# Optimization experiments

Hardware: AMD Instinct MI355X
Metric: run time of the kernel (lower is better)

The kernel has to match this reference:

```python
import jax, jax.numpy as jnp
import numpy as np

NUM_HEADS = 32
HEAD_DIM = 128
HIDDEN = NUM_HEADS * HEAD_DIM  # 4096
ROPE_BASE = 10000.0
VISION_TOKEN_TYPE = 1


def vision_expert_mask(token_type_ids):
    # vision_token_mask[:, :-1] = (tt[:, :-1]==1) & (tt[:, 1:]==1); last col False
    tt = token_type_ids
    m = (tt[:, :-1] == VISION_TOKEN_TYPE) & (tt[:, 1:] == VISION_TOKEN_TYPE)
    return jnp.concatenate([m, jnp.zeros((tt.shape[0], 1), dtype=bool)], axis=1)


def rotary_cos_sin(position_ids, head_dim, dtype):
    inv_freq = 1.0 / (ROPE_BASE ** (jnp.arange(0, head_dim, 2, dtype=jnp.float32) / head_dim))
    freqs = position_ids.astype(jnp.float32)[..., None] * inv_freq  # [B,S,Dh/2]
    emb = jnp.concatenate([freqs, freqs], axis=-1)  # [B,S,Dh]
    return jnp.cos(emb).astype(dtype), jnp.sin(emb).astype(dtype)


def rotate_half(x):
    d = x.shape[-1] // 2
    return jnp.concatenate([-x[..., d:], x[..., :d]], axis=-1)


def setup_inputs() -> dict:
    key = jax.random.key(0)
    ks = jax.random.split(key, 5)
    B, S = 2, 2048
    hidden_states = jax.random.normal(ks[0], (B, S, HIDDEN), dtype=jnp.float32)
    token_type_ids = jax.random.randint(ks[1], (B, S), 0, 2, dtype=jnp.int64)
    position_ids = jnp.broadcast_to(jnp.arange(S, dtype=jnp.int64)[None, :], (B, S))
    scale = 0.02
    w_vis_qkv = jax.random.normal(ks[2], (HIDDEN, 3 * HIDDEN), dtype=jnp.float32) * scale
    w_lang_qkv = jax.random.normal(ks[3], (HIDDEN, 3 * HIDDEN), dtype=jnp.float32) * scale
    w_vis_dense = jax.random.normal(ks[4], (HIDDEN, HIDDEN), dtype=jnp.float32) * scale
    w_lang_dense = jax.random.normal(jax.random.fold_in(key, 7), (HIDDEN, HIDDEN), dtype=jnp.float32) * scale
    return dict(hidden_states=hidden_states, token_type_ids=token_type_ids,
                position_ids=position_ids, w_vis_qkv=w_vis_qkv, w_lang_qkv=w_lang_qkv,
                w_vis_dense=w_vis_dense, w_lang_dense=w_lang_dense)


def reference(hidden_states, token_type_ids, position_ids,
              w_vis_qkv, w_lang_qkv, w_vis_dense, w_lang_dense):
    B, S, D = hidden_states.shape
    vm = vision_expert_mask(token_type_ids)  # [B,S] bool

    # 2-expert QKV dispatch (mask-select between the two expert GEMMs)
    qkv = jnp.where(vm[..., None],
                    hidden_states @ w_vis_qkv,
                    hidden_states @ w_lang_qkv)  # [B,S,3D]
    q, k, v = jnp.split(qkv, 3, axis=-1)
    q = q.reshape(B, S, NUM_HEADS, HEAD_DIM)
    k = k.reshape(B, S, NUM_HEADS, HEAD_DIM)
    v = v.reshape(B, S, NUM_HEADS, HEAD_DIM)

    # rotary embedding on q, k
    cos, sin = rotary_cos_sin(position_ids, HEAD_DIM, q.dtype)  # [B,S,Dh]
    cos, sin = cos[:, :, None, :], sin[:, :, None, :]
    q = q * cos + rotate_half(q) * sin
    k = k * cos + rotate_half(k) * sin

    # causal attention (dense equivalent of the paged-attention call)
    scores = jnp.einsum('bqhd,bkhd->bhqk', q, k) / jnp.sqrt(jnp.array(HEAD_DIM, q.dtype))
    causal = jnp.tril(jnp.ones((S, S), dtype=bool))
    scores = jnp.where(causal[None, None], scores, jnp.finfo(scores.dtype).min)
    probs = jax.nn.softmax(scores, axis=-1)
    ctx = jnp.einsum('bhqk,bkhd->bqhd', probs, v).reshape(B, S, D)

    # 2-expert output dense dispatch
    attn_output = jnp.where(vm[..., None],
                            ctx @ w_vis_dense,
                            ctx @ w_lang_dense)
    return attn_output
```

## Files before the change

kernel.cpp:

```cpp
#include <hip/hip_runtime.h>
#include <math.h>

#define SEQ     2048
#define NB      2
#define NHEADS  32
#define DHEAD   128
#define HID     4096
#define NQKV    12288
#define T_TOKENS (NB*SEQ)

typedef _Float16 half8 __attribute__((ext_vector_type(8)));
typedef float v4f __attribute__((ext_vector_type(4)));

__device__ __forceinline__ void gload_lds16(const void* g, void* l) {
    __builtin_amdgcn_global_load_lds(
        (__attribute__((address_space(1))) void*)(void*)(g),
        (__attribute__((address_space(3))) void*)(unsigned)(unsigned long long)(l),
        16, 0, 0);
}

__device__ __forceinline__ v4f mfma16(half8 a, half8 b, v4f c) {
    return __builtin_amdgcn_mfma_f32_16x16x32_f16(a, b, c, 0, 0, 0);
}

__global__ void route_kernel(const int* __restrict__ tt, int* counts, int* idx) {
    int t = blockIdx.x * blockDim.x + threadIdx.x;
    if (t >= T_TOKENS) return;
    int s = t & (SEQ - 1);
    bool vm = (s < SEQ - 1) && (tt[t] == 1) && (tt[t + 1] == 1);
    int e = vm ? 0 : 1;
    int p = atomicAdd(&counts[e], 1);
    idx[e * T_TOKENS + p] = t;
}

__global__ void rope_table_kernel(const int* __restrict__ pos_ids, float2* __restrict__ tab) {
    int i = blockIdx.x * blockDim.x + threadIdx.x;
    if (i >= T_TOKENS * 64) return;
    int tok = i >> 6, j = i & 63;
    float invf = (float)pow(10000.0, -(double)j * (1.0 / 64.0));
    float ang = (float)pos_ids[tok] * invf;
    double ds, dc;
    sincos((double)ang, &ds, &dc);
    tab[i] = make_float2((float)dc, (float)ds);
}

__global__ void cvt_f32_f16(const float* __restrict__ src, _Float16* __restrict__ dst, int n4) {
    int i = blockIdx.x * blockDim.x + threadIdx.x;
    if (i >= n4) return;
    float4 v = ((const float4*)src)[i];
    union { _Float16 h[4]; uint2 u; } p;
    p.h[0] = (_Float16)v.x; p.h[1] = (_Float16)v.y;
    p.h[2] = (_Float16)v.z; p.h[3] = (_Float16)v.w;
    ((uint2*)dst)[i] = p.u;
}

__global__ void transpose_cvt(const float* __restrict__ W, _Float16* __restrict__ WT,
                              int K, int N) {
    __shared__ _Float16 t[64][72];
    const int n0 = blockIdx.x * 64, k0 = blockIdx.y * 64;
    const int cr = threadIdx.x & 15, rr = threadIdx.x >> 4;
#pragma unroll
    for (int it = 0; it < 4; ++it) {
        int r = rr + it * 16;
        float4 v = *(const float4*)&W[(size_t)(k0 + r) * N + n0 + cr * 4];
        t[cr*4+0][r] = (_Float16)v.x; t[cr*4+1][r] = (_Float16)v.y;
        t[cr*4+2][r] = (_Float16)v.z; t[cr*4+3][r] = (_Float16)v.w;
    }
    __syncthreads();
#pragma unroll
    for (int it = 0; it < 4; ++it) {
        int r = rr + it * 16;
        union { _Float16 h[4]; uint2 u; } p;
#pragma unroll
        for (int j = 0; j < 4; ++j) p.h[j] = t[r][cr*4+j];
        *(uint2*)&WT[(size_t)(n0 + r) * K + k0 + cr * 4] = p.u;
    }
}

__global__ void transpose_v(const _Float16* __restrict__ vin, _Float16* __restrict__ vout) {
    __shared__ _Float16 t[64][72];
    const int s0 = blockIdx.x * 64;
    const int d0 = blockIdx.y * 64;
    const int bh = blockIdx.z;
    const int b = bh >> 5, h = bh & 31;
    const int cr = threadIdx.x & 15, rr = threadIdx.x >> 4;
#pragma unroll
    for (int it = 0; it < 4; ++it) {
        int sl = rr + it * 16;
        union { _Float16 h4[4]; uint2 u; } p;
        p.u = *(const uint2*)&vin[(size_t)(b * SEQ + s0 + sl) * HID + h * DHEAD + d0 + cr * 4];
#pragma unroll
        for (int j = 0; j < 4; ++j) t[cr*4+j][sl] = p.h4[j];
    }
    __syncthreads();
#pragma unroll
    for (int it = 0; it < 4; ++it) {
        int dl = rr + it * 16;
        union { _Float16 h4[4]; uint2 u; } p;
#pragma unroll
        for (int j = 0; j < 4; ++j) p.h4[j] = t[dl][cr*4+j];
        *(uint2*)&vout[((size_t)bh * DHEAD + d0 + dl) * SEQ + s0 + cr * 4] = p.u;
    }
}

template <int MODE>
__global__ __launch_bounds__(256, 2)
void gemm_expert(const _Float16* __restrict__ A,
                 const _Float16* __restrict__ BT0,
                 const _Float16* __restrict__ BT1,
                 const int* __restrict__ counts,
                 const int* __restrict__ idx_all,
                 const float2* __restrict__ rope,
                 _Float16* __restrict__ qbuf,
                 _Float16* __restrict__ kbuf,
                 _Float16* __restrict__ vbuf,
                 float* __restrict__ out) {
    const int e = blockIdx.z;
    const int count = counts[e];
    const int rt = blockIdx.y;
    if (rt * 128 >= count) return;
    const int ct = blockIdx.x;
    const int* idx = idx_all + e * T_TOKENS;
    const _Float16* BT = e ? BT1 : BT0;

    __shared__ _Float16 sA[128 * 32];
    __shared__ _Float16 sB[128 * 32];

    const int tid = threadIdx.x;
    const int w = tid >> 6, lane = tid & 63;
    const int col = lane & 15, quad = lane >> 4;

    const int r0 = (w * 2 + 0) * 16 + (lane >> 2);
    const int r1 = (w * 2 + 1) * 16 + (lane >> 2);
    int g0 = rt * 128 + r0; if (g0 > count - 1) g0 = count - 1;
    int g1 = rt * 128 + r1; if (g1 > count - 1) g1 = count - 1;
    const int tok0 = idx[g0], tok1 = idx[g1];
    const _Float16* ag0 = A + (size_t)tok0 * HID + (lane & 3) * 8;
    const _Float16* ag1 = A + (size_t)tok1 * HID + (lane & 3) * 8;
    const _Float16* bg0 = BT + (size_t)(ct * 128 + r0) * HID + (lane & 3) * 8;
    const _Float16* bg1 = BT + (size_t)(ct * 128 + r1) * HID + (lane & 3) * 8;
    _Float16* sa0 = &sA[(w * 2 + 0) * 512];
    _Float16* sa1 = &sA[(w * 2 + 1) * 512];
    _Float16* sb0 = &sB[(w * 2 + 0) * 512];
    _Float16* sb1 = &sB[(w * 2 + 1) * 512];

    v4f acc[2][8];
#pragma unroll
    for (int i = 0; i < 2; ++i)
#pragma unroll
        for (int j = 0; j < 8; ++j) { v4f z = {0.f, 0.f, 0.f, 0.f}; acc[i][j] = z; }

    const int am0 = (w * 32 + col) * 32 + quad * 8;
    const int am1 = am0 + 16 * 32;

    for (int kt = 0; kt < HID / 32; ++kt) {
        __syncthreads();
        gload_lds16(ag0, sa0); gload_lds16(ag1, sa1);
        gload_lds16(bg0, sb0); gload_lds16(bg1, sb1);
        ag0 += 32; ag1 += 32; bg0 += 32; bg1 += 32;
        __syncthreads();
        half8 a0 = *(const half8*)&sA[am0];
        half8 a1 = *(const half8*)&sA[am1];
#pragma unroll
        for (int nt = 0; nt < 8; ++nt) {
            half8 b = *(const half8*)&sB[(nt * 16 + col) * 32 + quad * 8];
            acc[0][nt] = mfma16(a0, b, acc[0][nt]);
            acc[1][nt] = mfma16(a1, b, acc[1][nt]);
        }
    }

    const int n0 = ct * 128;
    if (MODE == 1) {
#pragma unroll
        for (int mt = 0; mt < 2; ++mt)
#pragma unroll
            for (int r = 0; r < 4; ++r) {
                int rg = rt * 128 + w * 32 + mt * 16 + quad * 4 + r;
                if (rg >= count) continue;
                int tok = idx[rg];
                float* dst = out + (size_t)tok * HID + n0;
#pragma unroll
                for (int nt = 0; nt < 8; ++nt) dst[nt * 16 + col] = acc[mt][nt][r];
            }
    } else {
        const int sec = n0 >> 12;
        const int h = (n0 >> 7) & 31;
#pragma unroll
        for (int mt = 0; mt < 2; ++mt)
#pragma unroll
            for (int r = 0; r < 4; ++r) {
                int rg = rt * 128 + w * 32 + mt * 16 + quad * 4 + r;
                if (rg >= count) continue;
                int tok = idx[rg];
                int b = tok >> 11, s = tok & (SEQ - 1);
                if (sec == 2) {
                    _Float16* dst = vbuf + (size_t)tok * HID + h * DHEAD;
#pragma unroll
                    for (int nt = 0; nt < 8; ++nt) dst[nt * 16 + col] = (_Float16)acc[mt][nt][r];
                } else {
                    _Float16* dst = (sec ? kbuf : qbuf) + ((size_t)(b * NHEADS + h) * SEQ + s) * DHEAD;
                    const float2* tp = rope + (size_t)tok * 64;
#pragma unroll
                    for (int nt = 0; nt < 4; ++nt) {
                        int d = nt * 16 + col;
                        float2 cs = tp[d];
                        float x = acc[mt][nt][r], y = acc[mt][nt + 4][r];
                        dst[d]      = (_Float16)(x * cs.x - y * cs.y);
                        dst[d + 64] = (_Float16)(y * cs.x + x * cs.y);
                    }
                }
            }
    }
}

__global__ __launch_bounds__(256, 2)
void attn_kernel(const _Float16* __restrict__ qbuf,
                 const _Float16* __restrict__ kbuf,
                 const _Float16* __restrict__ vt,
                 _Float16* __restrict__ ctx) {
    const int f   = blockIdx.x;
    const int xcd = f & 7;
    const int t   = f >> 3;
    const int s   = t & 31;
    const int rr  = t >> 5;
    const int u   = s & 15, g = s >> 4;
    const int bh  = xcd * 8 + rr * 2 + g;
    const int qt  = (rr & 1) ? (15 - u) : u;

    const int b = bh >> 5, h = bh & 31;
    const int tid = threadIdx.x;
    const int w = tid >> 6, lane = tid & 63;
    const int col = lane & 15, quad = lane >> 4;

    __shared__ _Float16 sK[2][64 * 128];
    __shared__ _Float16 sV[2][128 * 64];
    __shared__ _Float16 sP[128 * 64];

    half8 qf[2][4];
    const _Float16 qscale = (_Float16)0.08838834764831845f;
#pragma unroll
    for (int mt = 0; mt < 2; ++mt)
#pragma unroll
        for (int kc = 0; kc < 4; ++kc) {
            int row = qt * 128 + w * 32 + mt * 16 + col;
            half8 v = *(const half8*)&qbuf[((size_t)bh * SEQ + row) * DHEAD + kc * 32 + quad * 8];
            qf[mt][kc] = v * qscale;
        }

    float mrow[2][4], lrow[2][4];
    v4f o[2][8];
#pragma unroll
    for (int mt = 0; mt < 2; ++mt)
#pragma unroll
        for (int r = 0; r < 4; ++r) { mrow[mt][r] = -3.0e38f; lrow[mt][r] = 0.f; }
#pragma unroll
    for (int i = 0; i < 2; ++i)
#pragma unroll
        for (int j = 0; j < 8; ++j) { v4f z = {0.f, 0.f, 0.f, 0.f}; o[i][j] = z; }

    const int cxor = col & 7;
    const int vs_chk = (lane & 7) ^ (lane >> 3);
    const int nkt = 2 * qt + 2;

    const _Float16* kg0 = kbuf + (size_t)bh * SEQ * DHEAD;
    const _Float16* vg0 = vt + (size_t)bh * DHEAD * SEQ;

    auto stage = [&](int kt, int buf) {
        const _Float16* kg = kg0 + (size_t)kt * 64 * DHEAD;
        const _Float16* vg = vg0 + kt * 64;
#pragma unroll
        for (int op = 0; op < 4; ++op) {
            int r0 = (w * 4 + op) * 4;
            int krow = r0 + quad;
            int kcs = col ^ (krow & 7);
            gload_lds16(kg + (size_t)krow * DHEAD + kcs * 8, &sK[buf][r0 * 128]);
            int d0 = (w * 4 + op) * 8;
            int vrow = d0 + (lane >> 3);
            gload_lds16(vg + (size_t)vrow * SEQ + vs_chk * 8, &sV[buf][d0 * 64]);
        }
    };

    stage(0, 0);
    __syncthreads();

    for (int kt = 0; kt < nkt; ++kt) {
        const int cur = kt & 1;
        if (kt + 1 < nkt) stage(kt + 1, cur ^ 1);

        v4f sc[2][4];
#pragma unroll
        for (int i = 0; i < 2; ++i)
#pragma unroll
            for (int j = 0; j < 4; ++j) { v4f z = {0.f, 0.f, 0.f, 0.f}; sc[i][j] = z; }
#pragma unroll
        for (int kc = 0; kc < 4; ++kc) {
            const int kof = ((kc * 4 + quad) ^ cxor) * 8;
#pragma unroll
            for (int nt = 0; nt < 4; ++nt) {
                half8 bf = *(const half8*)&sK[cur][(size_t)(nt * 16 + col) * 128 + kof];
                sc[0][nt] = mfma16(qf[0][kc], bf, sc[0][nt]);
                sc[1][nt] = mfma16(qf[1][kc], bf, sc[1][nt]);
            }
        }

        if (kt >= 2 * qt) {
#pragma unroll
            for (int mt = 0; mt < 2; ++mt)
#pragma unroll
                for (int nt = 0; nt < 4; ++nt)
#pragma unroll
                    for (int r = 0; r < 4; ++r) {
                        int rowa = qt * 128 + w * 32 + mt * 16 + quad * 4 + r;
                        int cola = kt * 64 + nt * 16 + col;
                        if (cola > rowa) sc[mt][nt][r] = -3.0e38f;
                    }
        }

#pragma unroll
        for (int mt = 0; mt < 2; ++mt)
#pragma unroll
            for (int r = 0; r < 4; ++r) {
                float mx = sc[mt][0][r];
#pragma unroll
                for (int nt = 1; nt < 4; ++nt) mx = fmaxf(mx, sc[mt][nt][r]);
                mx = fmaxf(mx, __shfl_xor(mx, 1));
                mx = fmaxf(mx, __shfl_xor(mx, 2));
                mx = fmaxf(mx, __shfl_xor(mx, 4));
                mx = fmaxf(mx, __shfl_xor(mx, 8));
                float newm = fmaxf(mrow[mt][r], mx);
                float alpha = __expf(mrow[mt][r] - newm);
                mrow[mt][r] = newm;
                float rs = 0.f;
#pragma unroll
                for (int nt = 0; nt < 4; ++nt) {
                    float p = __expf(sc[mt][nt][r] - newm);
                    sc[mt][nt][r] = p;
                    rs += p;
                }
                rs += __shfl_xor(rs, 1); rs += __shfl_xor(rs, 2);
                rs += __shfl_xor(rs, 4); rs += __shfl_xor(rs, 8);
                lrow[mt][r] = lrow[mt][r] * alpha + rs;
#pragma unroll
                for (int nt = 0; nt < 8; ++nt) o[mt][nt][r] *= alpha;
            }

#pragma unroll
        for (int mt = 0; mt < 2; ++mt)
#pragma unroll
            for (int nt = 0; nt < 4; ++nt)
#pragma unroll
                for (int r = 0; r < 4; ++r) {
                    int rp = w * 32 + mt * 16 + quad * 4 + r;
                    int colh = nt * 16 + col;
                    int c = (colh >> 3) ^ (rp & 7);
                    sP[(size_t)rp * 64 + c * 8 + (colh & 7)] = (_Float16)sc[mt][nt][r];
                }

#pragma unroll
        for (int kc = 0; kc < 2; ++kc) {
            const int kof = ((kc * 4 + quad) ^ cxor) * 8;
            half8 p0 = *(const half8*)&sP[(size_t)(w * 32 + col) * 64 + kof];
            half8 p1 = *(const half8*)&sP[(size_t)(w * 32 + 16 + col) * 64 + kof];
#pragma unroll
            for (int nt = 0; nt < 8; ++nt) {
                half8 vf = *(const half8*)&sV[cur][(size_t)(nt * 16 + col) * 64 + kof];
                o[0][nt] = mfma16(p0, vf, o[0][nt]);
                o[1][nt] = mfma16(p1, vf, o[1][nt]);
            }
        }

        __syncthreads();
    }

#pragma unroll
    for (int mt = 0; mt < 2; ++mt)
#pragma unroll
        for (int r = 0; r < 4; ++r) {
            int rowa = qt * 128 + w * 32 + mt * 16 + quad * 4 + r;
            float inv = 1.0f / lrow[mt][r];
            _Float16* dst = ctx + ((size_t)b * SEQ + rowa) * HID + h * DHEAD;
#pragma unroll
            for (int nt = 0; nt < 8; ++nt)
                dst[nt * 16 + col] = (_Float16)(o[mt][nt][r] * inv);
        }
}

extern "C" void kernel_launch(void* const* d_in, const int* in_sizes, int n_in,
                              void* d_out, int out_size, void* d_ws, size_t ws_size,
                              hipStream_t stream) {
    const float* hidden = (const float*)d_in[0];
    const int*   tt     = (const int*)d_in[1];
    const int*   pos    = (const int*)d_in[2];
    const float* wvq    = (const float*)d_in[3];
    const float* wlq    = (const float*)d_in[4];
    const float* wvd    = (const float*)d_in[5];
    const float* wld    = (const float*)d_in[6];
    float* out = (float*)d_out;

    char* ws = (char*)d_ws;
    size_t off = 0;
    auto alloc = [&](size_t bytes) {
        char* p = ws + off;
        off += (bytes + 255) & ~(size_t)255;
        return p;
    };
    const size_t TOKB = (size_t)T_TOKENS * HID * sizeof(_Float16);
    _Float16* h16  = (_Float16*)alloc(TOKB);
    _Float16* wvqT = (_Float16*)alloc((size_t)NQKV * HID * 2);
    _Float16* wlqT = (_Float16*)alloc((size_t)NQKV * HID * 2);
    _Float16* wvdT = (_Float16*)alloc((size_t)HID * HID * 2);
    _Float16* wldT = (_Float16*)alloc((size_t)HID * HID * 2);
    _Float16* qb   = (_Float16*)alloc(TOKB);
    _Float16* kb   = (_Float16*)alloc(TOKB);
    _Float16* vtmp = (_Float16*)alloc(TOKB);
    int* counts = (int*)alloc(2 * sizeof(int));
    int* idx    = (int*)alloc(2 * T_TOKENS * sizeof(int));
    float2* rope = (float2*)alloc((size_t)T_TOKENS * 64 * sizeof(float2));
    _Float16* vT  = h16;
    _Float16* ctx = vtmp;

    hipMemsetAsync(counts, 0, 2 * sizeof(int), stream);
    route_kernel<<<T_TOKENS / 256, 256, 0, stream>>>(tt, counts, idx);
    rope_table_kernel<<<(T_TOKENS * 64) / 256, 256, 0, stream>>>(pos, rope);
    cvt_f32_f16<<<(T_TOKENS * HID / 4) / 256, 256, 0, stream>>>(hidden, h16, T_TOKENS * HID / 4);
    transpose_cvt<<<dim3(NQKV / 64, HID / 64), 256, 0, stream>>>(wvq, wvqT, HID, NQKV);
    transpose_cvt<<<dim3(NQKV / 64, HID / 64), 256, 0, stream>>>(wlq, wlqT, HID, NQKV);
    transpose_cvt<<<dim3(HID / 64, HID / 64), 256, 0, stream>>>(wvd, wvdT, HID, HID);
    transpose_cvt<<<dim3(HID / 64, HID / 64), 256, 0, stream>>>(wld, wldT, HID, HID);
    gemm_expert<0><<<dim3(NQKV / 128, T_TOKENS / 128, 2), 256, 0, stream>>>(
        h16, wvqT, wlqT, counts, idx, rope, qb, kb, vtmp, nullptr);
    transpose_v<<<dim3(SEQ / 64, DHEAD / 64, NB * NHEADS), 256, 0, stream>>>(vtmp, vT);
    attn_kernel<<<dim3(16 * NB * NHEADS), 256, 0, stream>>>(qb, kb, vT, ctx);
    gemm_expert<1><<<dim3(HID / 128, T_TOKENS / 128, 2), 256, 0, stream>>>(
        ctx, wvdT, wldT, counts, idx, nullptr, nullptr, nullptr, nullptr, out);
}
```

Baseline: 1.650 ms.

## Double-buffer LDS in expert GEMM and remap blocks per XCD

The expert GEMM now stages A and B tiles in two LDS buffers. The next k-tile is issued before the MFMAs on the current one, and the loop uses one barrier per iteration instead of two, so global loads can overlap compute. It also remaps the flat block index so that the blocks on each XCD share a small group of column tiles, meant to improve L2 reuse of the weight tiles. The cost is double the LDS footprint. If the compiler inserts a conservative vmcnt wait before the LDS reads, little overlap may actually happen.

```diff
diff --git a/kernel.cpp b/kernel.cpp
--- a/kernel.cpp
+++ b/kernel.cpp
@@ -103,7 +103,7 @@
     }
 }
 
-template <int MODE>
+template <int MODE, int NCT>
 __global__ __launch_bounds__(256, 2)
 void gemm_expert(const _Float16* __restrict__ A,
                  const _Float16* __restrict__ BT0,
@@ -117,14 +117,21 @@
                  float* __restrict__ out) {
     const int e = blockIdx.z;
     const int count = counts[e];
-    const int rt = blockIdx.y;
+
+    const int f   = blockIdx.x + NCT * blockIdx.y;
+    const int xcd = f & 7;
+    const int g   = f >> 3;
+    const int c   = g >> 6;
+    const int wi  = g & 63;
+    const int rt  = wi >> 1;
+    const int ct  = xcd * (NCT / 8) + c * 2 + (wi & 1);
+
     if (rt * 128 >= count) return;
-    const int ct = blockIdx.x;
     const int* idx = idx_all + e * T_TOKENS;
     const _Float16* BT = e ? BT1 : BT0;
 
-    __shared__ _Float16 sA[128 * 32];
-    __shared__ _Float16 sB[128 * 32];
+    __shared__ _Float16 sA[2][128 * 32];
+    __shared__ _Float16 sB[2][128 * 32];
 
     const int tid = threadIdx.x;
     const int w = tid >> 6, lane = tid & 63;
@@ -139,10 +146,8 @@
     const _Float16* ag1 = A + (size_t)tok1 * HID + (lane & 3) * 8;
     const _Float16* bg0 = BT + (size_t)(ct * 128 + r0) * HID + (lane & 3) * 8;
     const _Float16* bg1 = BT + (size_t)(ct * 128 + r1) * HID + (lane & 3) * 8;
-    _Float16* sa0 = &sA[(w * 2 + 0) * 512];
-    _Float16* sa1 = &sA[(w * 2 + 1) * 512];
-    _Float16* sb0 = &sB[(w * 2 + 0) * 512];
-    _Float16* sb1 = &sB[(w * 2 + 1) * 512];
+    const int sa_off0 = (w * 2 + 0) * 512;
+    const int sa_off1 = (w * 2 + 1) * 512;
 
     v4f acc[2][8];
 #pragma unroll
@@ -153,20 +158,27 @@
     const int am0 = (w * 32 + col) * 32 + quad * 8;
     const int am1 = am0 + 16 * 32;
 
+    gload_lds16(ag0, &sA[0][sa_off0]); gload_lds16(ag1, &sA[0][sa_off1]);
+    gload_lds16(bg0, &sB[0][sa_off0]); gload_lds16(bg1, &sB[0][sa_off1]);
+    ag0 += 32; ag1 += 32; bg0 += 32; bg1 += 32;
+    __syncthreads();
+
     for (int kt = 0; kt < HID / 32; ++kt) {
-        __syncthreads();
-        gload_lds16(ag0, sa0); gload_lds16(ag1, sa1);
-        gload_lds16(bg0, sb0); gload_lds16(bg1, sb1);
-        ag0 += 32; ag1 += 32; bg0 += 32; bg1 += 32;
-        __syncthreads();
-        half8 a0 = *(const half8*)&sA[am0];
-        half8 a1 = *(const half8*)&sA[am1];
+        const int cur = kt & 1, nxt = cur ^ 1;
+        if (kt + 1 < HID / 32) {
+            gload_lds16(ag0, &sA[nxt][sa_off0]); gload_lds16(ag1, &sA[nxt][sa_off1]);
+            gload_lds16(bg0, &sB[nxt][sa_off0]); gload_lds16(bg1, &sB[nxt][sa_off1]);
+            ag0 += 32; ag1 += 32; bg0 += 32; bg1 += 32;
+        }
+        half8 a0 = *(const half8*)&sA[cur][am0];
+        half8 a1 = *(const half8*)&sA[cur][am1];
 #pragma unroll
         for (int nt = 0; nt < 8; ++nt) {
-            half8 b = *(const half8*)&sB[(nt * 16 + col) * 32 + quad * 8];
+            half8 b = *(const half8*)&sB[cur][(nt * 16 + col) * 32 + quad * 8];
             acc[0][nt] = mfma16(a0, b, acc[0][nt]);
             acc[1][nt] = mfma16(a1, b, acc[1][nt]);
         }
+        __syncthreads();
     }
 
     const int n0 = ct * 128;
@@ -427,10 +439,10 @@
     transpose_cvt<<<dim3(NQKV / 64, HID / 64), 256, 0, stream>>>(wlq, wlqT, HID, NQKV);
     transpose_cvt<<<dim3(HID / 64, HID / 64), 256, 0, stream>>>(wvd, wvdT, HID, HID);
     transpose_cvt<<<dim3(HID / 64, HID / 64), 256, 0, stream>>>(wld, wldT, HID, HID);
-    gemm_expert<0><<<dim3(NQKV / 128, T_TOKENS / 128, 2), 256, 0, stream>>>(
+    gemm_expert<0, NQKV / 128><<<dim3(NQKV / 128, T_TOKENS / 128, 2), 256, 0, stream>>>(
         h16, wvqT, wlqT, counts, idx, rope, qb, kb, vtmp, nullptr);
     transpose_v<<<dim3(SEQ / 64, DHEAD / 64, NB * NHEADS), 256, 0, stream>>>(vtmp, vT);
     attn_kernel<<<dim3(16 * NB * NHEADS), 256, 0, stream>>>(qb, kb, vT, ctx);
-    gemm_expert<1><<<dim3(HID / 128, T_TOKENS / 128, 2), 256, 0, stream>>>(
+    gemm_expert<1, HID / 128><<<dim3(HID / 128, T_TOKENS / 128, 2), 256, 0, stream>>>(
         ctx, wvdT, wldT, counts, idx, nullptr, nullptr, nullptr, nullptr, out);
 }
```

New measurement: 1.613 ms. 1.02x faster.
